# Kernel optimization log

Measured on AMD Instinct MI355X. Metric: run time of the kernel, lower is better.

The kernel has to match this reference:

```python
import jax, jax.numpy as jnp
import numpy as np

# --- instant-NGP style multiresolution hash grid config ---
N_LEVELS = 16
F = 2                      # features per level
LOG2_T = 19
T = 1 << LOG2_T            # hash table size per level
BASE_RES = 16
SCALE = 1.5
RES = np.floor(BASE_RES * SCALE ** np.arange(N_LEVELS)).astype(np.int64)
OFFSETS = np.array([[i, j, k] for i in (0, 1) for j in (0, 1) for k in (0, 1)], dtype=np.uint32)  # [8,3] cube corners
PRIMES = np.array([1, 2654435761, 805459861], dtype=np.uint32)  # tcnn spatial hash primes
N_PTS = 2_097_152


def hash_encode(x, table):
    """x: [N,3] in [0,1); table: [L,T,F] -> [N, L*F] interpolated features."""
    feats = []
    for l in range(N_LEVELS):  # fixed small loop over levels
        res = int(RES[l])
        pos = x * res
        pos0 = jnp.floor(pos)
        w = pos - pos0                                   # [N,3] trilinear weights
        c = pos0.astype(jnp.uint32)[:, None, :] + OFFSETS[None]  # [N,8,3] corner coords
        if (res + 1) ** 3 <= T:
            # dense indexing when the full grid fits in the table
            s = np.uint32(res + 1)
            idx = c[..., 0] + c[..., 1] * s + c[..., 2] * s * s
        else:
            # spatial hash: xor of coord * prime, mod T (uint32 wraps)
            idx = (c[..., 0] * PRIMES[0]) ^ (c[..., 1] * PRIMES[1]) ^ (c[..., 2] * PRIMES[2])
            idx = idx % np.uint32(T)
        f = table[l][idx]                                # [N,8,F] irregular gather
        wc = jnp.where(OFFSETS[None].astype(bool), w[:, None, :], 1.0 - w[:, None, :])  # [N,8,3]
        weight = wc.prod(axis=-1)                        # [N,8]
        feats.append(jnp.einsum('nc,ncf->nf', weight, f))
    return jnp.concatenate(feats, axis=-1)               # [N, 32]


def setup_inputs() -> dict:
    key = jax.random.key(0)
    k1, k2, k3, k4, k5 = jax.random.split(key, 5)
    x = jax.random.uniform(k1, (N_PTS, 3), dtype=jnp.float32)
    table = jax.random.normal(k2, (N_LEVELS, T, F), dtype=jnp.float32) * 1e-2
    W1 = jax.random.normal(k3, (N_LEVELS * F, 64), dtype=jnp.float32) * (1.0 / np.sqrt(32))
    W2 = jax.random.normal(k4, (64, 64), dtype=jnp.float32) * (1.0 / 8.0)
    W3 = jax.random.normal(k5, (64, 16), dtype=jnp.float32) * (1.0 / 8.0)
    return {"x": x, "table": table, "W1": W1, "W2": W2, "W3": W3}


def reference(x, table, W1, W2, W3):
    h = hash_encode(x, table)           # [N,32]
    h = jax.nn.relu(h @ W1)             # fully-fused tiny MLP (bias-free, tcnn style)
    h = jax.nn.relu(h @ W2)
    return h @ W3                        # [N,16]
```

## Files before the change

### kernel.cpp

```cpp
#include <hip/hip_runtime.h>
#include <hip/hip_bf16.h>


#define NLVL 16
#define TSZ   524288u
#define TMASK 524287u
#define PR1 2654435761u
#define PR2 805459861u

__device__ __constant__ int kResC[NLVL] = {16,24,36,54,81,121,182,273,410,615,922,1383,2075,3113,4670,7006};
constexpr int kRes[NLVL] = {16,24,36,54,81,121,182,273,410,615,922,1383,2075,3113,4670,7006};
constexpr bool kDense[NLVL] = {true,true,true,true,false,false,false,false,
                               false,false,false,false,false,false,false,false};


__device__ __forceinline__ void trilerp(const float2 f0, const float2 f1, const float2 f2, const float2 f3,
                                        const float2 f4, const float2 f5, const float2 f6, const float2 f7,
                                        float wx, float wy, float wz, float& a0, float& a1)
{
    const float ax = 1.f - wx, ay = 1.f - wy, az = 1.f - wz;
    const float g00 = ax * ay, g01 = ax * wy, g10 = wx * ay, g11 = wx * wy;
    float s0 = 0.f, s1 = 0.f, v;
    v = g00 * az; s0 = fmaf(v, f0.x, s0); s1 = fmaf(v, f0.y, s1);
    v = g00 * wz; s0 = fmaf(v, f1.x, s0); s1 = fmaf(v, f1.y, s1);
    v = g01 * az; s0 = fmaf(v, f2.x, s0); s1 = fmaf(v, f2.y, s1);
    v = g01 * wz; s0 = fmaf(v, f3.x, s0); s1 = fmaf(v, f3.y, s1);
    v = g10 * az; s0 = fmaf(v, f4.x, s0); s1 = fmaf(v, f4.y, s1);
    v = g10 * wz; s0 = fmaf(v, f5.x, s0); s1 = fmaf(v, f5.y, s1);
    v = g11 * az; s0 = fmaf(v, f6.x, s0); s1 = fmaf(v, f6.y, s1);
    v = g11 * wz; s0 = fmaf(v, f7.x, s0); s1 = fmaf(v, f7.y, s1);
    a0 = s0; a1 = s1;
}

__device__ __forceinline__ void hash_point(float px, float py, float pz, float res,
                                           const float2* __restrict__ tl,
                                           float& a0, float& a1)
{
    const float fx = px * res, fy = py * res, fz = pz * res;
    const float bx = floorf(fx), by = floorf(fy), bz = floorf(fz);
    const float wx = fx - bx, wy = fy - by, wz = fz - bz;
    const unsigned cx = (unsigned)bx, cy = (unsigned)by, cz = (unsigned)bz;
    const unsigned hy0 = cy * PR1, hy1 = hy0 + PR1;
    const unsigned hz0 = cz * PR2, hz1 = hz0 + PR2;
    const unsigned e00 = hy0 ^ hz0, e01 = hy0 ^ hz1, e10 = hy1 ^ hz0, e11 = hy1 ^ hz1;
    const unsigned x1 = cx + 1u;
    const float2 f0 = tl[(cx ^ e00) & TMASK];
    const float2 f1 = tl[(cx ^ e01) & TMASK];
    const float2 f2 = tl[(cx ^ e10) & TMASK];
    const float2 f3 = tl[(cx ^ e11) & TMASK];
    const float2 f4 = tl[(x1 ^ e00) & TMASK];
    const float2 f5 = tl[(x1 ^ e01) & TMASK];
    const float2 f6 = tl[(x1 ^ e10) & TMASK];
    const float2 f7 = tl[(x1 ^ e11) & TMASK];
    trilerp(f0,f1,f2,f3,f4,f5,f6,f7, wx,wy,wz, a0,a1);
}

template<int RES>
__device__ __forceinline__ void dense_point(float px, float py, float pz,
                                            const float2* __restrict__ tl,
                                            float& a0, float& a1)
{
    const float res = (float)RES;
    const float fx = px * res, fy = py * res, fz = pz * res;
    const float bx = floorf(fx), by = floorf(fy), bz = floorf(fz);
    const float wx = fx - bx, wy = fy - by, wz = fz - bz;
    const unsigned cx = (unsigned)bx, cy = (unsigned)by, cz = (unsigned)bz;
    const unsigned s = RES + 1u, s2 = s * s;
    const unsigned b = cx + cy * s + cz * s2;
    const float2 f0 = tl[b];
    const float2 f1 = tl[b + s2];
    const float2 f2 = tl[b + s];
    const float2 f3 = tl[b + s + s2];
    const float2 f4 = tl[b + 1u];
    const float2 f5 = tl[b + 1u + s2];
    const float2 f6 = tl[b + 1u + s];
    const float2 f7 = tl[b + 1u + s + s2];
    trilerp(f0,f1,f2,f3,f4,f5,f6,f7, wx,wy,wz, a0,a1);
}

__global__ __launch_bounds__(256)
void encode_kernel(const float* __restrict__ x, const float* __restrict__ table,
                   float* __restrict__ hT, int n)
{
    const int bid = blockIdx.x;
    const int pass = bid >> 12;
    const int chunk = bid & 4095;
    const int t = threadIdx.x;
    const int base = chunk * 512 + t;

    if (pass == 0) {
#pragma unroll
        for (int p = 0; p < 2; ++p) {
            const int i = base + p * 256;
            if (i >= n) continue;
            const float px = x[3*i+0], py = x[3*i+1], pz = x[3*i+2];
            float a0, a1;
            dense_point<16>(px,py,pz, (const float2*)table + (size_t)0*TSZ, a0,a1);
            hT[(size_t)0*n + i] = a0; hT[(size_t)1*n + i] = a1;
            dense_point<24>(px,py,pz, (const float2*)table + (size_t)1*TSZ, a0,a1);
            hT[(size_t)2*n + i] = a0; hT[(size_t)3*n + i] = a1;
            dense_point<36>(px,py,pz, (const float2*)table + (size_t)2*TSZ, a0,a1);
            hT[(size_t)4*n + i] = a0; hT[(size_t)5*n + i] = a1;
            dense_point<54>(px,py,pz, (const float2*)table + (size_t)3*TSZ, a0,a1);
            hT[(size_t)6*n + i] = a0; hT[(size_t)7*n + i] = a1;
        }
    } else {
        const int l = pass + 3;
        const float res = (float)kResC[l];
        const float2* tl = (const float2*)table + (size_t)l * TSZ;
        float* __restrict__ r0 = hT + (size_t)(2*l) * n;
        float* __restrict__ r1 = r0 + n;
#pragma unroll
        for (int p = 0; p < 2; ++p) {
            const int i = base + p * 256;
            if (i >= n) continue;
            const float px = x[3*i+0], py = x[3*i+1], pz = x[3*i+2];
            float a0, a1;
            hash_point(px,py,pz, res, tl, a0,a1);
            r0[i] = a0; r1[i] = a1;
        }
    }
}


__global__ __launch_bounds__(256)
void mlp_kernel(const float* __restrict__ hT,
                const float* __restrict__ W1,
                const float* __restrict__ W2,
                const float* __restrict__ W3,
                float* __restrict__ out, int n)
{
    __shared__ float sW1[32 * 64];
    __shared__ float sW2[64 * 64];
    __shared__ float sW3[64 * 16];
    const int t = threadIdx.x;
#pragma unroll
    for (int r = 0; r < 8; ++r)  sW1[r * 256 + t] = W1[r * 256 + t];
#pragma unroll
    for (int r = 0; r < 16; ++r) sW2[r * 256 + t] = W2[r * 256 + t];
#pragma unroll
    for (int r = 0; r < 4; ++r)  sW3[r * 256 + t] = W3[r * 256 + t];
    __syncthreads();

    const int i = blockIdx.x * 256 + t;
    if (i >= n) return;

    float h[32];
#pragma unroll
    for (int f = 0; f < 32; ++f) h[f] = hT[(size_t)f * n + i];

    float h1[64];
#pragma unroll
    for (int j = 0; j < 64; ++j) h1[j] = 0.f;
#pragma unroll
    for (int k = 0; k < 32; ++k) {
        const float hk = h[k];
        const float4* __restrict__ wr = reinterpret_cast<const float4*>(&sW1[k * 64]);
#pragma unroll
        for (int q = 0; q < 16; ++q) {
            const float4 wv = wr[q];
            h1[4*q+0] = fmaf(hk, wv.x, h1[4*q+0]);
            h1[4*q+1] = fmaf(hk, wv.y, h1[4*q+1]);
            h1[4*q+2] = fmaf(hk, wv.z, h1[4*q+2]);
            h1[4*q+3] = fmaf(hk, wv.w, h1[4*q+3]);
        }
    }
#pragma unroll
    for (int j = 0; j < 64; ++j) h1[j] = fmaxf(h1[j], 0.f);

    float h3[16];
#pragma unroll
    for (int j = 0; j < 16; ++j) h3[j] = 0.f;

#pragma unroll
    for (int half = 0; half < 2; ++half) {
        float h2[32];
#pragma unroll
        for (int j = 0; j < 32; ++j) h2[j] = 0.f;
#pragma unroll
        for (int k = 0; k < 64; ++k) {
            const float hk = h1[k];
            const float4* __restrict__ wr = reinterpret_cast<const float4*>(&sW2[k * 64 + half * 32]);
#pragma unroll
            for (int q = 0; q < 8; ++q) {
                const float4 wv = wr[q];
                h2[4*q+0] = fmaf(hk, wv.x, h2[4*q+0]);
                h2[4*q+1] = fmaf(hk, wv.y, h2[4*q+1]);
                h2[4*q+2] = fmaf(hk, wv.z, h2[4*q+2]);
                h2[4*q+3] = fmaf(hk, wv.w, h2[4*q+3]);
            }
        }
#pragma unroll
        for (int j = 0; j < 32; ++j) h2[j] = fmaxf(h2[j], 0.f);
#pragma unroll
        for (int k = 0; k < 32; ++k) {
            const float hk = h2[k];
            const float4* __restrict__ wr = reinterpret_cast<const float4*>(&sW3[(half * 32 + k) * 16]);
#pragma unroll
            for (int q = 0; q < 4; ++q) {
                const float4 wv = wr[q];
                h3[4*q+0] = fmaf(hk, wv.x, h3[4*q+0]);
                h3[4*q+1] = fmaf(hk, wv.y, h3[4*q+1]);
                h3[4*q+2] = fmaf(hk, wv.z, h3[4*q+2]);
                h3[4*q+3] = fmaf(hk, wv.w, h3[4*q+3]);
            }
        }
    }

    float4* __restrict__ o = reinterpret_cast<float4*>(out + (size_t)i * 16);
    o[0] = make_float4(h3[0],  h3[1],  h3[2],  h3[3]);
    o[1] = make_float4(h3[4],  h3[5],  h3[6],  h3[7]);
    o[2] = make_float4(h3[8],  h3[9],  h3[10], h3[11]);
    o[3] = make_float4(h3[12], h3[13], h3[14], h3[15]);
}


__global__ __launch_bounds__(256)
void ngp_fused_kernel(const float* __restrict__ x,
                      const float* __restrict__ table,
                      const float* __restrict__ W1,
                      const float* __restrict__ W2,
                      const float* __restrict__ W3,
                      float* __restrict__ out,
                      int n)
{
    __shared__ float sW1[32 * 64];
    __shared__ float sW2[64 * 64];
    __shared__ float sW3[64 * 16];
    __shared__ float hS[32 * 256];

    const int t = threadIdx.x;
#pragma unroll
    for (int r = 0; r < 8; ++r)  sW1[r * 256 + t] = W1[r * 256 + t];
#pragma unroll
    for (int r = 0; r < 16; ++r) sW2[r * 256 + t] = W2[r * 256 + t];
#pragma unroll
    for (int r = 0; r < 4; ++r)  sW3[r * 256 + t] = W3[r * 256 + t];
    __syncthreads();

    const int i = blockIdx.x * 256 + t;
    if (i >= n) return;

    const float px = x[3*i+0], py = x[3*i+1], pz = x[3*i+2];

    float h[32];
#pragma unroll
    for (int l = 0; l < NLVL; ++l) {
        float a0, a1;
        if (kDense[l]) {
            const int r = kRes[l];
            if (r == 16) dense_point<16>(px,py,pz,(const float2*)table+(size_t)l*TSZ,a0,a1);
            else if (r == 24) dense_point<24>(px,py,pz,(const float2*)table+(size_t)l*TSZ,a0,a1);
            else if (r == 36) dense_point<36>(px,py,pz,(const float2*)table+(size_t)l*TSZ,a0,a1);
            else dense_point<54>(px,py,pz,(const float2*)table+(size_t)l*TSZ,a0,a1);
        } else {
            hash_point(px,py,pz,(float)kRes[l],(const float2*)table+(size_t)l*TSZ,a0,a1);
        }
        h[2*l+0] = a0; h[2*l+1] = a1;
    }

#pragma unroll
    for (int k = 0; k < 32; ++k) hS[k * 256 + t] = h[k];

    float h1[64];
#pragma unroll
    for (int j = 0; j < 64; ++j) h1[j] = 0.f;
    for (int k = 0; k < 32; ++k) {
        const float hk = hS[k * 256 + t];
        const float4* __restrict__ wr = reinterpret_cast<const float4*>(&sW1[k * 64]);
#pragma unroll
        for (int q = 0; q < 16; ++q) {
            const float4 wv = wr[q];
            h1[4*q+0] = fmaf(hk, wv.x, h1[4*q+0]);
            h1[4*q+1] = fmaf(hk, wv.y, h1[4*q+1]);
            h1[4*q+2] = fmaf(hk, wv.z, h1[4*q+2]);
            h1[4*q+3] = fmaf(hk, wv.w, h1[4*q+3]);
        }
    }
#pragma unroll
    for (int j = 0; j < 64; ++j) h1[j] = fmaxf(h1[j], 0.f);

    float h2[64];
#pragma unroll
    for (int j = 0; j < 64; ++j) h2[j] = 0.f;
#pragma unroll
    for (int half = 0; half < 2; ++half) {
#pragma unroll
        for (int k = 0; k < 32; ++k) hS[k * 256 + t] = h1[half * 32 + k];
        for (int k = 0; k < 32; ++k) {
            const float hk = hS[k * 256 + t];
            const float4* __restrict__ wr = reinterpret_cast<const float4*>(&sW2[(half * 32 + k) * 64]);
#pragma unroll
            for (int q = 0; q < 16; ++q) {
                const float4 wv = wr[q];
                h2[4*q+0] = fmaf(hk, wv.x, h2[4*q+0]);
                h2[4*q+1] = fmaf(hk, wv.y, h2[4*q+1]);
                h2[4*q+2] = fmaf(hk, wv.z, h2[4*q+2]);
                h2[4*q+3] = fmaf(hk, wv.w, h2[4*q+3]);
            }
        }
    }
#pragma unroll
    for (int j = 0; j < 64; ++j) h2[j] = fmaxf(h2[j], 0.f);

    float h3[16];
#pragma unroll
    for (int j = 0; j < 16; ++j) h3[j] = 0.f;
#pragma unroll
    for (int half = 0; half < 2; ++half) {
#pragma unroll
        for (int k = 0; k < 32; ++k) hS[k * 256 + t] = h2[half * 32 + k];
        for (int k = 0; k < 32; ++k) {
            const float hk = hS[k * 256 + t];
            const float4* __restrict__ wr = reinterpret_cast<const float4*>(&sW3[(half * 32 + k) * 16]);
#pragma unroll
            for (int q = 0; q < 4; ++q) {
                const float4 wv = wr[q];
                h3[4*q+0] = fmaf(hk, wv.x, h3[4*q+0]);
                h3[4*q+1] = fmaf(hk, wv.y, h3[4*q+1]);
                h3[4*q+2] = fmaf(hk, wv.z, h3[4*q+2]);
                h3[4*q+3] = fmaf(hk, wv.w, h3[4*q+3]);
            }
        }
    }

    float4* __restrict__ o = reinterpret_cast<float4*>(out + (size_t)i * 16);
    o[0] = make_float4(h3[0],  h3[1],  h3[2],  h3[3]);
    o[1] = make_float4(h3[4],  h3[5],  h3[6],  h3[7]);
    o[2] = make_float4(h3[8],  h3[9],  h3[10], h3[11]);
    o[3] = make_float4(h3[12], h3[13], h3[14], h3[15]);
}

extern "C" void kernel_launch(void* const* d_in, const int* in_sizes, int n_in,
                              void* d_out, int out_size, void* d_ws, size_t ws_size,
                              hipStream_t stream) {
    const float* x     = (const float*)d_in[0];
    const float* table = (const float*)d_in[1];
    const float* W1    = (const float*)d_in[2];
    const float* W2    = (const float*)d_in[3];
    const float* W3    = (const float*)d_in[4];
    float* out = (float*)d_out;

    const int n = in_sizes[0] / 3;
    const size_t need = (size_t)n * 32 * sizeof(float);

    if (ws_size >= need) {
        float* hT = (float*)d_ws;
        const int chunks = (n + 511) / 512;
        encode_kernel<<<13 * 4096, 256, 0, stream>>>(x, table, hT, n);
        (void)chunks;
        mlp_kernel<<<(n + 255) / 256, 256, 0, stream>>>(hT, W1, W2, W3, out, n);
    } else {
        ngp_fused_kernel<<<(n + 255) / 256, 256, 0, stream>>>(x, table, W1, W2, W3, out, n);
    }
}
```

Baseline: 1.741 ms.

## Split dense/hash encode kernels, batch 4 points per thread, read MLP weights from global

The combined encode kernel is split into a dense-level kernel and a hash-level kernel. The hash kernel processes four points per thread, using vectorized float4 loads for coordinates and outputs and issuing all 32 gathers before interpolating, to raise memory-level parallelism. The MLP kernel now uses 64-thread blocks and reads weights straight from global memory (uniform, cache-resident) instead of staging them in LDS, and it stages activations through LDS to save registers. The intent is to cut gather latency and LDS/occupancy limits, at the cost of more register pressure in the hash kernel and relying on the scalar/L1 cache for weights.

```diff
diff --git a/kernel.cpp b/kernel.cpp
--- a/kernel.cpp
+++ b/kernel.cpp
@@ -12,7 +12,6 @@
 constexpr int kRes[NLVL] = {16,24,36,54,81,121,182,273,410,615,922,1383,2075,3113,4670,7006};
 constexpr bool kDense[NLVL] = {true,true,true,true,false,false,false,false,
                                false,false,false,false,false,false,false,false};
-
 
 __device__ __forceinline__ void trilerp(const float2 f0, const float2 f1, const float2 f2, const float2 f3,
                                         const float2 f4, const float2 f5, const float2 f6, const float2 f7,
@@ -79,126 +78,156 @@
 }
 
 __global__ __launch_bounds__(256)
-void encode_kernel(const float* __restrict__ x, const float* __restrict__ table,
-                   float* __restrict__ hT, int n)
-{
-    const int bid = blockIdx.x;
-    const int pass = bid >> 12;
-    const int chunk = bid & 4095;
-    const int t = threadIdx.x;
-    const int base = chunk * 512 + t;
-
-    if (pass == 0) {
-#pragma unroll
-        for (int p = 0; p < 2; ++p) {
-            const int i = base + p * 256;
-            if (i >= n) continue;
-            const float px = x[3*i+0], py = x[3*i+1], pz = x[3*i+2];
+void encode_dense(const float* __restrict__ x, const float* __restrict__ table,
+                  float* __restrict__ hT, int n)
+{
+    const int i = blockIdx.x * 256 + threadIdx.x;
+    if (i >= n) return;
+    const float px = x[3*i+0], py = x[3*i+1], pz = x[3*i+2];
+    const float2* tb = (const float2*)table;
+    float a0, a1;
+    dense_point<16>(px,py,pz, tb,              a0,a1);
+    hT[i] = a0;                     hT[(size_t)n + i] = a1;
+    dense_point<24>(px,py,pz, tb + TSZ,        a0,a1);
+    hT[(size_t)2*n + i] = a0;       hT[(size_t)3*n + i] = a1;
+    dense_point<36>(px,py,pz, tb + 2*(size_t)TSZ, a0,a1);
+    hT[(size_t)4*n + i] = a0;       hT[(size_t)5*n + i] = a1;
+    dense_point<54>(px,py,pz, tb + 3*(size_t)TSZ, a0,a1);
+    hT[(size_t)6*n + i] = a0;       hT[(size_t)7*n + i] = a1;
+}
+
+__global__ __launch_bounds__(256)
+void encode_hash(const float* __restrict__ x, const float* __restrict__ table,
+                 float* __restrict__ hT, int n, int chunks)
+{
+    const int bid  = blockIdx.x;
+    const int pass = bid / chunks;
+    const int chunk = bid - pass * chunks;
+    const int l = pass + 4;
+    const float res = (float)kResC[l];
+    const float2* __restrict__ tl = (const float2*)table + (size_t)l * TSZ;
+    float* __restrict__ r0 = hT + (size_t)(2*l) * n;
+    float* __restrict__ r1 = r0 + n;
+
+    const int t  = threadIdx.x;
+    const int i0 = (chunk << 10) + (t << 2);
+
+    if (i0 + 3 < n) {
+        const float4* __restrict__ xv = reinterpret_cast<const float4*>(x + (size_t)3 * i0);
+        const float4 A = xv[0], B = xv[1], C = xv[2];
+        const float px[4] = {A.x, A.w, B.z, C.y};
+        const float py[4] = {A.y, B.x, B.w, C.z};
+        const float pz[4] = {A.z, B.y, C.x, C.w};
+
+        unsigned idx[4][8];
+        float wx[4], wy[4], wz[4];
+#pragma unroll
+        for (int p = 0; p < 4; ++p) {
+            const float fx = px[p]*res, fy = py[p]*res, fz = pz[p]*res;
+            const float bx = floorf(fx), by = floorf(fy), bz = floorf(fz);
+            wx[p] = fx - bx; wy[p] = fy - by; wz[p] = fz - bz;
+            const unsigned cx = (unsigned)bx, cy = (unsigned)by, cz = (unsigned)bz;
+            const unsigned hy0 = cy * PR1, hy1 = hy0 + PR1;
+            const unsigned hz0 = cz * PR2, hz1 = hz0 + PR2;
+            const unsigned e00 = hy0 ^ hz0, e01 = hy0 ^ hz1, e10 = hy1 ^ hz0, e11 = hy1 ^ hz1;
+            const unsigned x1c = cx + 1u;
+            idx[p][0] = (cx  ^ e00) & TMASK;  idx[p][1] = (cx  ^ e01) & TMASK;
+            idx[p][2] = (cx  ^ e10) & TMASK;  idx[p][3] = (cx  ^ e11) & TMASK;
+            idx[p][4] = (x1c ^ e00) & TMASK;  idx[p][5] = (x1c ^ e01) & TMASK;
+            idx[p][6] = (x1c ^ e10) & TMASK;  idx[p][7] = (x1c ^ e11) & TMASK;
+        }
+        float2 f[4][8];
+#pragma unroll
+        for (int p = 0; p < 4; ++p)
+#pragma unroll
+            for (int c = 0; c < 8; ++c) f[p][c] = tl[idx[p][c]];
+
+        float o0[4], o1[4];
+#pragma unroll
+        for (int p = 0; p < 4; ++p)
+            trilerp(f[p][0],f[p][1],f[p][2],f[p][3],f[p][4],f[p][5],f[p][6],f[p][7],
+                    wx[p],wy[p],wz[p], o0[p],o1[p]);
+
+        *reinterpret_cast<float4*>(r0 + i0) = make_float4(o0[0],o0[1],o0[2],o0[3]);
+        *reinterpret_cast<float4*>(r1 + i0) = make_float4(o1[0],o1[1],o1[2],o1[3]);
+    } else {
+#pragma unroll
+        for (int p = 0; p < 4; ++p) {
+            const int i = i0 + p;
+            if (i >= n) break;
+            const float qx = x[3*i+0], qy = x[3*i+1], qz = x[3*i+2];
             float a0, a1;
-            dense_point<16>(px,py,pz, (const float2*)table + (size_t)0*TSZ, a0,a1);
-            hT[(size_t)0*n + i] = a0; hT[(size_t)1*n + i] = a1;
-            dense_point<24>(px,py,pz, (const float2*)table + (size_t)1*TSZ, a0,a1);
-            hT[(size_t)2*n + i] = a0; hT[(size_t)3*n + i] = a1;
-            dense_point<36>(px,py,pz, (const float2*)table + (size_t)2*TSZ, a0,a1);
-            hT[(size_t)4*n + i] = a0; hT[(size_t)5*n + i] = a1;
-            dense_point<54>(px,py,pz, (const float2*)table + (size_t)3*TSZ, a0,a1);
-            hT[(size_t)6*n + i] = a0; hT[(size_t)7*n + i] = a1;
-        }
-    } else {
-        const int l = pass + 3;
-        const float res = (float)kResC[l];
-        const float2* tl = (const float2*)table + (size_t)l * TSZ;
-        float* __restrict__ r0 = hT + (size_t)(2*l) * n;
-        float* __restrict__ r1 = r0 + n;
-#pragma unroll
-        for (int p = 0; p < 2; ++p) {
-            const int i = base + p * 256;
-            if (i >= n) continue;
-            const float px = x[3*i+0], py = x[3*i+1], pz = x[3*i+2];
-            float a0, a1;
-            hash_point(px,py,pz, res, tl, a0,a1);
+            hash_point(qx,qy,qz, res, tl, a0,a1);
             r0[i] = a0; r1[i] = a1;
         }
     }
 }
 
-
-__global__ __launch_bounds__(256)
+__global__ __launch_bounds__(64)
 void mlp_kernel(const float* __restrict__ hT,
                 const float* __restrict__ W1,
                 const float* __restrict__ W2,
                 const float* __restrict__ W3,
                 float* __restrict__ out, int n)
 {
-    __shared__ float sW1[32 * 64];
-    __shared__ float sW2[64 * 64];
-    __shared__ float sW3[64 * 16];
+    __shared__ float hS[32 * 64];
     const int t = threadIdx.x;
-#pragma unroll
-    for (int r = 0; r < 8; ++r)  sW1[r * 256 + t] = W1[r * 256 + t];
-#pragma unroll
-    for (int r = 0; r < 16; ++r) sW2[r * 256 + t] = W2[r * 256 + t];
-#pragma unroll
-    for (int r = 0; r < 4; ++r)  sW3[r * 256 + t] = W3[r * 256 + t];
-    __syncthreads();
-
-    const int i = blockIdx.x * 256 + t;
+    const int i = blockIdx.x * 64 + t;
     if (i >= n) return;
 
-    float h[32];
-#pragma unroll
-    for (int f = 0; f < 32; ++f) h[f] = hT[(size_t)f * n + i];
+#pragma unroll
+    for (int f = 0; f < 32; ++f) hS[f * 64 + t] = hT[(size_t)f * n + i];
 
     float h1[64];
 #pragma unroll
     for (int j = 0; j < 64; ++j) h1[j] = 0.f;
-#pragma unroll
     for (int k = 0; k < 32; ++k) {
-        const float hk = h[k];
-        const float4* __restrict__ wr = reinterpret_cast<const float4*>(&sW1[k * 64]);
+        const float hk = hS[k * 64 + t];
+        const float* __restrict__ Wr = W1 + k * 64;
 #pragma unroll
         for (int q = 0; q < 16; ++q) {
-            const float4 wv = wr[q];
+            const float4 wv = *reinterpret_cast<const float4*>(Wr + 4*q);
             h1[4*q+0] = fmaf(hk, wv.x, h1[4*q+0]);
             h1[4*q+1] = fmaf(hk, wv.y, h1[4*q+1]);
             h1[4*q+2] = fmaf(hk, wv.z, h1[4*q+2]);
             h1[4*q+3] = fmaf(hk, wv.w, h1[4*q+3]);
         }
     }
-#pragma unroll
-    for (int j = 0; j < 64; ++j) h1[j] = fmaxf(h1[j], 0.f);
-
-    float h3[16];
-#pragma unroll
-    for (int j = 0; j < 16; ++j) h3[j] = 0.f;
-
+
+    float h2[64];
+#pragma unroll
+    for (int j = 0; j < 64; ++j) h2[j] = 0.f;
 #pragma unroll
     for (int half = 0; half < 2; ++half) {
-        float h2[32];
-#pragma unroll
-        for (int j = 0; j < 32; ++j) h2[j] = 0.f;
-#pragma unroll
-        for (int k = 0; k < 64; ++k) {
-            const float hk = h1[k];
-            const float4* __restrict__ wr = reinterpret_cast<const float4*>(&sW2[k * 64 + half * 32]);
-#pragma unroll
-            for (int q = 0; q < 8; ++q) {
-                const float4 wv = wr[q];
+#pragma unroll
+        for (int k = 0; k < 32; ++k) hS[k * 64 + t] = fmaxf(h1[half*32 + k], 0.f);
+        for (int k = 0; k < 32; ++k) {
+            const float hk = hS[k * 64 + t];
+            const float* __restrict__ Wr = W2 + (half*32 + k) * 64;
+#pragma unroll
+            for (int q = 0; q < 16; ++q) {
+                const float4 wv = *reinterpret_cast<const float4*>(Wr + 4*q);
                 h2[4*q+0] = fmaf(hk, wv.x, h2[4*q+0]);
                 h2[4*q+1] = fmaf(hk, wv.y, h2[4*q+1]);
                 h2[4*q+2] = fmaf(hk, wv.z, h2[4*q+2]);
                 h2[4*q+3] = fmaf(hk, wv.w, h2[4*q+3]);
             }
         }
-#pragma unroll
-        for (int j = 0; j < 32; ++j) h2[j] = fmaxf(h2[j], 0.f);
-#pragma unroll
+    }
+
+    float h3[16];
+#pragma unroll
+    for (int j = 0; j < 16; ++j) h3[j] = 0.f;
+#pragma unroll
+    for (int half = 0; half < 2; ++half) {
+#pragma unroll
+        for (int k = 0; k < 32; ++k) hS[k * 64 + t] = fmaxf(h2[half*32 + k], 0.f);
         for (int k = 0; k < 32; ++k) {
-            const float hk = h2[k];
-            const float4* __restrict__ wr = reinterpret_cast<const float4*>(&sW3[(half * 32 + k) * 16]);
+            const float hk = hS[k * 64 + t];
+            const float* __restrict__ Wr = W3 + (half*32 + k) * 16;
 #pragma unroll
             for (int q = 0; q < 4; ++q) {
-                const float4 wv = wr[q];
+                const float4 wv = *reinterpret_cast<const float4*>(Wr + 4*q);
                 h3[4*q+0] = fmaf(hk, wv.x, h3[4*q+0]);
                 h3[4*q+1] = fmaf(hk, wv.y, h3[4*q+1]);
                 h3[4*q+2] = fmaf(hk, wv.z, h3[4*q+2]);
@@ -213,7 +242,6 @@
     o[2] = make_float4(h3[8],  h3[9],  h3[10], h3[11]);
     o[3] = make_float4(h3[12], h3[13], h3[14], h3[15]);
 }
-
 
 __global__ __launch_bounds__(256)
 void ngp_fused_kernel(const float* __restrict__ x,
@@ -224,23 +252,10 @@
                       float* __restrict__ out,
                       int n)
 {
-    __shared__ float sW1[32 * 64];
-    __shared__ float sW2[64 * 64];
-    __shared__ float sW3[64 * 16];
     __shared__ float hS[32 * 256];
-
     const int t = threadIdx.x;
-#pragma unroll
-    for (int r = 0; r < 8; ++r)  sW1[r * 256 + t] = W1[r * 256 + t];
-#pragma unroll
-    for (int r = 0; r < 16; ++r) sW2[r * 256 + t] = W2[r * 256 + t];
-#pragma unroll
-    for (int r = 0; r < 4; ++r)  sW3[r * 256 + t] = W3[r * 256 + t];
-    __syncthreads();
-
     const int i = blockIdx.x * 256 + t;
     if (i >= n) return;
-
     const float px = x[3*i+0], py = x[3*i+1], pz = x[3*i+2];
 
     float h[32];
@@ -261,74 +276,60 @@
 
 #pragma unroll
     for (int k = 0; k < 32; ++k) hS[k * 256 + t] = h[k];
-
     float h1[64];
 #pragma unroll
     for (int j = 0; j < 64; ++j) h1[j] = 0.f;
     for (int k = 0; k < 32; ++k) {
         const float hk = hS[k * 256 + t];
-        const float4* __restrict__ wr = reinterpret_cast<const float4*>(&sW1[k * 64]);
+        const float* __restrict__ Wr = W1 + k * 64;
 #pragma unroll
         for (int q = 0; q < 16; ++q) {
-            const float4 wv = wr[q];
-            h1[4*q+0] = fmaf(hk, wv.x, h1[4*q+0]);
-            h1[4*q+1] = fmaf(hk, wv.y, h1[4*q+1]);
-            h1[4*q+2] = fmaf(hk, wv.z, h1[4*q+2]);
-            h1[4*q+3] = fmaf(hk, wv.w, h1[4*q+3]);
-        }
-    }
-#pragma unroll
-    for (int j = 0; j < 64; ++j) h1[j] = fmaxf(h1[j], 0.f);
-
+            const float4 wv = *reinterpret_cast<const float4*>(Wr + 4*q);
+            h1[4*q+0]=fmaf(hk,wv.x,h1[4*q+0]); h1[4*q+1]=fmaf(hk,wv.y,h1[4*q+1]);
+            h1[4*q+2]=fmaf(hk,wv.z,h1[4*q+2]); h1[4*q+3]=fmaf(hk,wv.w,h1[4*q+3]);
+        }
+    }
     float h2[64];
 #pragma unroll
     for (int j = 0; j < 64; ++j) h2[j] = 0.f;
 #pragma unroll
     for (int half = 0; half < 2; ++half) {
 #pragma unroll
-        for (int k = 0; k < 32; ++k) hS[k * 256 + t] = h1[half * 32 + k];
+        for (int k = 0; k < 32; ++k) hS[k * 256 + t] = fmaxf(h1[half*32+k], 0.f);
         for (int k = 0; k < 32; ++k) {
             const float hk = hS[k * 256 + t];
-            const float4* __restrict__ wr = reinterpret_cast<const float4*>(&sW2[(half * 32 + k) * 64]);
+            const float* __restrict__ Wr = W2 + (half*32+k) * 64;
 #pragma unroll
             for (int q = 0; q < 16; ++q) {
-                const float4 wv = wr[q];
-                h2[4*q+0] = fmaf(hk, wv.x, h2[4*q+0]);
-                h2[4*q+1] = fmaf(hk, wv.y, h2[4*q+1]);
-                h2[4*q+2] = fmaf(hk, wv.z, h2[4*q+2]);
-                h2[4*q+3] = fmaf(hk, wv.w, h2[4*q+3]);
+                const float4 wv = *reinterpret_cast<const float4*>(Wr + 4*q);
+                h2[4*q+0]=fmaf(hk,wv.x,h2[4*q+0]); h2[4*q+1]=fmaf(hk,wv.y,h2[4*q+1]);
+                h2[4*q+2]=fmaf(hk,wv.z,h2[4*q+2]); h2[4*q+3]=fmaf(hk,wv.w,h2[4*q+3]);
             }
         }
     }
-#pragma unroll
-    for (int j = 0; j < 64; ++j) h2[j] = fmaxf(h2[j], 0.f);
-
     float h3[16];
 #pragma unroll
     for (int j = 0; j < 16; ++j) h3[j] = 0.f;
 #pragma unroll
     for (int half = 0; half < 2; ++half) {
 #pragma unroll
-        for (int k = 0; k < 32; ++k) hS[k * 256 + t] = h2[half * 32 + k];
+        for (int k = 0; k < 32; ++k) hS[k * 256 + t] = fmaxf(h2[half*32+k], 0.f);
         for (int k = 0; k < 32; ++k) {
             const float hk = hS[k * 256 + t];
-            const float4* __restrict__ wr = reinterpret_cast<const float4*>(&sW3[(half * 32 + k) * 16]);
+            const float* __restrict__ Wr = W3 + (half*32+k) * 16;
 #pragma unroll
             for (int q = 0; q < 4; ++q) {
-                const float4 wv = wr[q];
-                h3[4*q+0] = fmaf(hk, wv.x, h3[4*q+0]);
-                h3[4*q+1] = fmaf(hk, wv.y, h3[4*q+1]);
-                h3[4*q+2] = fmaf(hk, wv.z, h3[4*q+2]);
-                h3[4*q+3] = fmaf(hk, wv.w, h3[4*q+3]);
+                const float4 wv = *reinterpret_cast<const float4*>(Wr + 4*q);
+                h3[4*q+0]=fmaf(hk,wv.x,h3[4*q+0]); h3[4*q+1]=fmaf(hk,wv.y,h3[4*q+1]);
+                h3[4*q+2]=fmaf(hk,wv.z,h3[4*q+2]); h3[4*q+3]=fmaf(hk,wv.w,h3[4*q+3]);
             }
         }
     }
-
     float4* __restrict__ o = reinterpret_cast<float4*>(out + (size_t)i * 16);
-    o[0] = make_float4(h3[0],  h3[1],  h3[2],  h3[3]);
-    o[1] = make_float4(h3[4],  h3[5],  h3[6],  h3[7]);
-    o[2] = make_float4(h3[8],  h3[9],  h3[10], h3[11]);
-    o[3] = make_float4(h3[12], h3[13], h3[14], h3[15]);
+    o[0] = make_float4(h3[0],h3[1],h3[2],h3[3]);
+    o[1] = make_float4(h3[4],h3[5],h3[6],h3[7]);
+    o[2] = make_float4(h3[8],h3[9],h3[10],h3[11]);
+    o[3] = make_float4(h3[12],h3[13],h3[14],h3[15]);
 }
 
 extern "C" void kernel_launch(void* const* d_in, const int* in_sizes, int n_in,
@@ -346,10 +347,10 @@
 
     if (ws_size >= need) {
         float* hT = (float*)d_ws;
-        const int chunks = (n + 511) / 512;
-        encode_kernel<<<13 * 4096, 256, 0, stream>>>(x, table, hT, n);
-        (void)chunks;
-        mlp_kernel<<<(n + 255) / 256, 256, 0, stream>>>(hT, W1, W2, W3, out, n);
+        encode_dense<<<(n + 255) / 256, 256, 0, stream>>>(x, table, hT, n);
+        const int chunks = (n + 1023) / 1024;
+        encode_hash<<<12 * chunks, 256, 0, stream>>>(x, table, hT, n, chunks);
+        mlp_kernel<<<(n + 63) / 64, 64, 0, stream>>>(hT, W1, W2, W3, out, n);
     } else {
         ngp_fused_kernel<<<(n + 255) / 256, 256, 0, stream>>>(x, table, W1, W2, W3, out, n);
     }
```

New measurement: 1.573 ms. 1.11x faster.
